# Optimization experiments

Measured on AMD Instinct MI355X. Metric: run time of the kernel, lower is better.

Reference implementation:

```python
import jax, jax.numpy as jnp
import numpy as np

B, S, E, H = 64, 512, 256, 512


def setup_inputs() -> dict:
    key = jax.random.key(0)
    ks = jax.random.split(key, 8)
    std_h = 1.0 / np.sqrt(H)
    std_e = 1.0 / np.sqrt(E)
    return {
        "inputs": jax.random.normal(ks[0], (B, S, E), dtype=jnp.float32),
        "timestamps": jax.random.uniform(ks[1], (B, S), dtype=jnp.float32) * 10.0,
        "W_all_w": jax.random.uniform(ks[2], (4 * H, H), jnp.float32, -std_h, std_h),
        "W_all_b": jax.random.uniform(ks[3], (4 * H,), jnp.float32, -std_h, std_h),
        "U_all_w": jax.random.uniform(ks[4], (4 * H, E), jnp.float32, -std_e, std_e),
        "U_all_b": jax.random.uniform(ks[5], (4 * H,), jnp.float32, -std_e, std_e),
        "W_d_w": jax.random.uniform(ks[6], (H, H), jnp.float32, -std_h, std_h),
        "W_d_b": jax.random.uniform(ks[7], (H,), jnp.float32, -std_h, std_h),
    }


def reference(inputs, timestamps, W_all_w, W_all_b, U_all_w, U_all_b, W_d_w, W_d_b):
    b, seq, embed = inputs.shape
    hidden = W_d_w.shape[0]
    # Precompute input projections for all steps: [b, seq, 4H]
    u_proj = jnp.einsum('bse,ge->bsg', inputs, U_all_w) + U_all_b
    # Time-decay factor per step: 1 / log(e + dt), shape [b, seq, 1]
    decay = (1.0 / jnp.log(jnp.float32(np.e) + timestamps))[..., None]

    def step(carry, xs):
        h, c = carry
        u_s, dec_s = xs  # [b, 4H], [b, 1]
        c_s1 = jnp.tanh(c @ W_d_w.T + W_d_b)
        c_adj = (c - c_s1) + c_s1 * dec_s
        outs = h @ W_all_w.T + W_all_b + u_s
        f, i, o, c_tmp = jnp.split(outs, 4, axis=1)
        f = jax.nn.sigmoid(f)
        i = jax.nn.sigmoid(i)
        o = jax.nn.sigmoid(o)
        c_tmp = jnp.tanh(c_tmp)
        c_new = f * c_adj + i * c_tmp
        h_new = o * jnp.tanh(c_new)
        return (h_new, c_new), h_new

    h0 = jnp.zeros((b, hidden), dtype=inputs.dtype)
    c0 = jnp.zeros((b, hidden), dtype=inputs.dtype)
    # scan over seq: move time to leading axis
    (h_f, c_f), hs = jax.lax.scan(
        step, (h0, c0),
        (jnp.swapaxes(u_proj, 0, 1), jnp.swapaxes(decay, 0, 1)))
    outputs = jnp.swapaxes(hs, 0, 1)  # [b, seq, H]
    return outputs, h_f, c_f
```

## Files before the change

kernel.cpp:

```cpp
#include <hip/hip_runtime.h>
#include <cmath>


typedef short bf16x8 __attribute__((ext_vector_type(8)));
typedef float f32x4  __attribute__((ext_vector_type(4)));

#define Bdim 64
#define Sdim 512
#define Edim 256
#define Hdim 512
#define NWG  64
#define NT   512
#define FSTR 16

#define WS_FLAGS 0
#define WS_HMIR0 16384
#define WS_HMIR1 (WS_HMIR0 + 65536)
#define WS_CMIR0 (WS_HMIR1 + 65536)
#define WS_CMIR1 (WS_CMIR0 + 65536)
#define WS_WFRAG (WS_CMIR1 + 65536)
#define WS_DFRAG (WS_WFRAG + 3145728)

__device__ __forceinline__ unsigned ld_dev_u32(const unsigned* p) {
    return __hip_atomic_load(p, __ATOMIC_RELAXED, __HIP_MEMORY_SCOPE_AGENT);
}
__device__ __forceinline__ void st_dev_u32(unsigned* p, unsigned v) {
    __hip_atomic_store(p, v, __ATOMIC_RELAXED, __HIP_MEMORY_SCOPE_AGENT);
}
__device__ __forceinline__ unsigned long long ld_dev_u64(const unsigned long long* p) {
    return __hip_atomic_load(p, __ATOMIC_RELAXED, __HIP_MEMORY_SCOPE_AGENT);
}
__device__ __forceinline__ unsigned short f2bf(float f) {
    union { float f; unsigned u; } v; v.f = f;
    return (unsigned short)((v.u + 0x7FFFu + ((v.u >> 16) & 1u)) >> 16);
}
__device__ __forceinline__ unsigned pack2(float lo, float hi) {
    return (unsigned)f2bf(lo) | ((unsigned)f2bf(hi) << 16);
}
__device__ __forceinline__ float fast_tanh(float x) {
    const float ax = __builtin_fabsf(x);
    const float e  = __expf(-2.0f * ax);
    const float t  = (1.0f - e) / (1.0f + e);
    return __builtin_copysignf(t, x);
}
__device__ __forceinline__ float fast_sigmoid(float x) {
    return 1.0f / (1.0f + __expf(-x));
}

__global__ __launch_bounds__(256) void tlstm_prep(
    const float* __restrict__ Wall, const float* __restrict__ Uall,
    const float* __restrict__ Wd, unsigned char* __restrict__ ws)
{
    const int w = blockIdx.x, t = threadIdx.x;
    unsigned short* Wfrag = (unsigned short*)(ws + WS_WFRAG);
    unsigned short* Dfrag = (unsigned short*)(ws + WS_DFRAG);
    const int l = t & 63, ks = t >> 6, nn = l & 15, q = l >> 4;

    if (w < 128) {
        const int cg = w >> 3, wv = w & 7;
        const int G = wv * 16 + nn, g = G >> 5, jj = G & 31;
        const int row = g * Hdim + cg * 32 + jj;
        for (int i = 0; i < 6; ++i) {
            const int kp = ks * 6 + i;
            const float* src = (kp < 16)
                ? Wall + (size_t)row * Hdim + kp * 32 + q * 8
                : Uall + (size_t)row * Edim + (kp - 16) * 32 + q * 8;
            unsigned* dst = (unsigned*)(Wfrag
                + (((size_t)(cg * 8 + wv) * 24 + kp) * 64 + l) * 8);
            #pragma unroll
            for (int p = 0; p < 4; ++p) dst[p] = pack2(src[2*p], src[2*p+1]);
        }
    } else if (w < 192) {
        const int u = w - 128, cg = u >> 2, q4 = u & 3;
        for (int half = 0; half < 2; ++half) {
            const int wv = q4 * 2 + half;
            const int i  = ks;
            const int dt = wv >> 2, kd = (wv & 3) * 4 + i;
            const int row = cg * 32 + dt * 16 + nn;
            const float* src = Wd + (size_t)row * Hdim + kd * 32 + q * 8;
            unsigned* dst = (unsigned*)(Dfrag
                + (((size_t)(cg * 8 + wv) * 4 + i) * 64 + l) * 8);
            #pragma unroll
            for (int p = 0; p < 4; ++p) dst[p] = pack2(src[2*p], src[2*p+1]);
        }
    } else {
        const int idx = (w - 192) * 256 + t;
        uint4* z = (uint4*)ws;
        for (int i = idx; i < 17408; i += 16384) z[i] = make_uint4(0, 0, 0, 0);
    }
}

__global__ __launch_bounds__(NT, 2) void tlstm_mfma(
    const float* __restrict__ x,
    const float* __restrict__ ts,
    const float* __restrict__ Wall_b,
    const float* __restrict__ Uall_b,
    const float* __restrict__ Wd_b,
    float* __restrict__ out,
    unsigned char* __restrict__ ws)
{
    __shared__ __align__(16) unsigned short h_sb[16 * 520];
    __shared__ __align__(16) unsigned short c_sb[16 * 520];
    __shared__ __align__(16) unsigned short x_sb[16 * 264];
    __shared__ float Dred[2][4][256];
    __shared__ float act[4 * 512];
    __shared__ float cs1v[512];
    __shared__ float decv[16];

    int* flags = (int*)(ws + WS_FLAGS);
    const unsigned short* Wfrag = (const unsigned short*)(ws + WS_WFRAG);
    const unsigned short* Dfrag = (const unsigned short*)(ws + WS_DFRAG);

    const int t    = threadIdx.x;
    const int bg   = blockIdx.x >> 4, cg = blockIdx.x & 15;
    const int b0   = bg * 16, j0 = cg * 32;
    const int w    = t >> 6, lane = t & 63, q = lane >> 4, nn = lane & 15;

    const int G = w * 16 + nn, g = G >> 5, jj = G & 31;
    const float bias_g = Wall_b[g * Hdim + j0 + jj] + Uall_b[g * Hdim + j0 + jj];
    const int rtl = t >> 8, rpos = t & 255, rm = rpos >> 4, rn = rpos & 15;
    const float bias_d = Wd_b[j0 + rtl * 16 + rn];
    const int fm = t >> 5, fj = t & 31;

    bf16x8 bw[24];
    #pragma unroll
    for (int i = 0; i < 24; ++i)
        bw[i] = *(const bf16x8*)(Wfrag
            + (((size_t)(cg * 8 + w) * 24 + i) * 64 + lane) * 8);
    bf16x8 bd[4];
    #pragma unroll
    for (int i = 0; i < 4; ++i)
        bd[i] = *(const bf16x8*)(Dfrag
            + (((size_t)(cg * 8 + w) * 4 + i) * 64 + lane) * 8);

    const int srow = t >> 5, sc32 = t & 31;

    auto stage_x = [&](int sx) {
        const float4* xp = (const float4*)(x + ((size_t)(b0 + srow) * Sdim + sx) * Edim + sc32 * 8);
        float4 v0 = xp[0], v1 = xp[1];
        *(uint4*)((unsigned*)x_sb + srow * 132 + sc32 * 4) =
            make_uint4(pack2(v0.x, v0.y), pack2(v0.z, v0.w),
                       pack2(v1.x, v1.y), pack2(v1.z, v1.w));
    };

    float c_reg = 0.0f;
    stage_x(0);

    for (int s = 0;; ++s) {
        {
            const unsigned long long* hsrc =
                (const unsigned long long*)(ws + WS_HMIR0 + (s & 1) * 65536);
            const unsigned long long* csrc =
                (const unsigned long long*)(ws + WS_CMIR0 + (s & 1) * 65536);
            const int goff = ((b0 + srow) * 256 + sc32 * 8) >> 1;
            unsigned long long hv[4], cv[4];
            #pragma unroll
            for (int i = 0; i < 4; ++i) hv[i] = ld_dev_u64(hsrc + goff + i);
            #pragma unroll
            for (int i = 0; i < 4; ++i) cv[i] = ld_dev_u64(csrc + goff + i);
            unsigned* hls = (unsigned*)h_sb + srow * 260 + sc32 * 8;
            unsigned* cls = (unsigned*)c_sb + srow * 260 + sc32 * 8;
            ((ulonglong2*)hls)[0] = make_ulonglong2(hv[0], hv[1]);
            ((ulonglong2*)hls)[1] = make_ulonglong2(hv[2], hv[3]);
            ((ulonglong2*)cls)[0] = make_ulonglong2(cv[0], cv[1]);
            ((ulonglong2*)cls)[1] = make_ulonglong2(cv[2], cv[3]);
        }
        __syncthreads();

        f32x4 acc0 = {0.f, 0.f, 0.f, 0.f}, acc1 = {0.f, 0.f, 0.f, 0.f};
        f32x4 accd = {0.f, 0.f, 0.f, 0.f};
        #pragma unroll
        for (int i = 0; i < 12; ++i) {
            bf16x8 av = *(const bf16x8*)(h_sb + nn * 520 + i * 32 + q * 8);
            acc0 = __builtin_amdgcn_mfma_f32_16x16x32_bf16(av, bw[i], acc0, 0, 0, 0);
        }
        #pragma unroll
        for (int i = 12; i < 24; ++i) {
            const unsigned short* asrc = (i < 16)
                ? (h_sb + nn * 520 + i * 32 + q * 8)
                : (x_sb + nn * 264 + (i - 16) * 32 + q * 8);
            bf16x8 av = *(const bf16x8*)asrc;
            acc1 = __builtin_amdgcn_mfma_f32_16x16x32_bf16(av, bw[i], acc1, 0, 0, 0);
        }
        #pragma unroll
        for (int i = 0; i < 4; ++i) {
            const int kd = (w & 3) * 4 + i;
            bf16x8 av = *(const bf16x8*)(c_sb + nn * 520 + kd * 32 + q * 8);
            accd = __builtin_amdgcn_mfma_f32_16x16x32_bf16(av, bd[i], accd, 0, 0, 0);
        }

        const int dt = w >> 2;
        #pragma unroll
        for (int r = 0; r < 4; ++r) {
            const int m = q * 4 + r;
            const float sv = acc0[r] + acc1[r] + bias_g;
            act[g * 512 + m * 32 + jj] = (g == 3) ? fast_tanh(sv) : fast_sigmoid(sv);
            Dred[dt][w & 3][m * 16 + ((nn + m) & 15)] = accd[r];
        }
        __syncthreads();

        {
            const int sl = rm * 16 + ((rn + rm) & 15);
            const float sv = Dred[rtl][0][sl] + Dred[rtl][1][sl]
                           + Dred[rtl][2][sl] + Dred[rtl][3][sl];
            cs1v[rm * 32 + rtl * 16 + rn] = fast_tanh(sv + bias_d);
        }
        if (t < 16)
            decv[t] = 1.0f / __logf(2.7182818284590452f + ts[(b0 + t) * Sdim + s]);
        __syncthreads();

        {
            const float dec  = decv[fm];
            const float cs1  = cs1v[t];
            const float cadj = (c_reg - cs1) + cs1 * dec;
            const float f  = act[t];
            const float ii = act[512 + t];
            const float oo = act[1024 + t];
            const float gg = act[1536 + t];
            const float cn = f * cadj + ii * gg;
            const float hn = oo * fast_tanh(cn);
            c_reg = cn;
            out[((size_t)(b0 + fm) * Sdim + s) * Hdim + j0 + fj] = hn;
            const float hn1 = __shfl_down(hn, 1);
            const float cn1 = __shfl_down(cn, 1);
            if (s < Sdim - 1) {
                if ((t & 1) == 0) {
                    unsigned* hmw = (unsigned*)(ws + WS_HMIR0 + ((s + 1) & 1) * 65536);
                    unsigned* cmw = (unsigned*)(ws + WS_CMIR0 + ((s + 1) & 1) * 65536);
                    const int didx = ((b0 + fm) * Hdim + j0 + fj) >> 1;
                    st_dev_u32(hmw + didx, pack2(hn, hn1));
                    st_dev_u32(cmw + didx, pack2(cn, cn1));
                }
            } else {
                float* hf = out + (size_t)Bdim * Sdim * Hdim;
                float* cf = hf + (size_t)Bdim * Hdim;
                hf[(b0 + fm) * Hdim + j0 + fj] = hn;
                cf[(b0 + fm) * Hdim + j0 + fj] = cn;
            }
        }

        if (s == Sdim - 1) break;

        __syncthreads();
        if (t == 0)
            __hip_atomic_store(&flags[blockIdx.x * FSTR], s + 1,
                               __ATOMIC_RELAXED, __HIP_MEMORY_SCOPE_AGENT);
        stage_x(s + 1);
        if (t < 16) {
            while (__hip_atomic_load(&flags[(bg * 16 + t) * FSTR],
                                     __ATOMIC_RELAXED,
                                     __HIP_MEMORY_SCOPE_AGENT) < s + 1) {
                __builtin_amdgcn_s_sleep(1);
            }
        }
        __syncthreads();
    }
}

extern "C" void kernel_launch(void* const* d_in, const int* in_sizes, int n_in,
                              void* d_out, int out_size, void* d_ws, size_t ws_size,
                              hipStream_t stream) {
    const float* x      = (const float*)d_in[0];
    const float* ts     = (const float*)d_in[1];
    const float* Wall   = (const float*)d_in[2];
    const float* Wall_b = (const float*)d_in[3];
    const float* Uall   = (const float*)d_in[4];
    const float* Uall_b = (const float*)d_in[5];
    const float* Wd     = (const float*)d_in[6];
    const float* Wd_b   = (const float*)d_in[7];

    tlstm_prep<<<256, 256, 0, stream>>>(Wall, Uall, Wd, (unsigned char*)d_ws);
    tlstm_mfma<<<NWG, NT, 0, stream>>>(x, ts, Wall_b, Uall_b, Wd_b,
                                       (float*)d_out, (unsigned char*)d_ws);
}
```

Measured before the change: 2.008 ms.

## Restructure per-step sync: per-producer flag waits, direct x MFMA, fewer barriers

```diff
diff --git a/kernel.cpp b/kernel.cpp
--- a/kernel.cpp
+++ b/kernel.cpp
@@ -99,13 +99,11 @@
     float* __restrict__ out,
     unsigned char* __restrict__ ws)
 {
-    __shared__ __align__(16) unsigned short h_sb[16 * 520];
-    __shared__ __align__(16) unsigned short c_sb[16 * 520];
-    __shared__ __align__(16) unsigned short x_sb[16 * 264];
+    __shared__ __align__(16) unsigned short h_sb[16 * 512];
+    __shared__ __align__(16) unsigned short c_sb[16 * 512];
     __shared__ float Dred[2][4][256];
     __shared__ float act[4 * 512];
-    __shared__ float cs1v[512];
-    __shared__ float decv[16];
+    __shared__ float dectab[16 * 512];
 
     int* flags = (int*)(ws + WS_FLAGS);
     const unsigned short* Wfrag = (const unsigned short*)(ws + WS_WFRAG);
@@ -118,9 +116,9 @@
 
     const int G = w * 16 + nn, g = G >> 5, jj = G & 31;
     const float bias_g = Wall_b[g * Hdim + j0 + jj] + Uall_b[g * Hdim + j0 + jj];
-    const int rtl = t >> 8, rpos = t & 255, rm = rpos >> 4, rn = rpos & 15;
-    const float bias_d = Wd_b[j0 + rtl * 16 + rn];
     const int fm = t >> 5, fj = t & 31;
+    const int fdt = fj >> 4, fn = fj & 15;
+    const float bias_d = Wd_b[j0 + fj];
 
     bf16x8 bw[24];
     #pragma unroll
@@ -134,58 +132,83 @@
             + (((size_t)(cg * 8 + w) * 4 + i) * 64 + lane) * 8);
 
     const int srow = t >> 5, sc32 = t & 31;
-
-    auto stage_x = [&](int sx) {
-        const float4* xp = (const float4*)(x + ((size_t)(b0 + srow) * Sdim + sx) * Edim + sc32 * 8);
-        float4 v0 = xp[0], v1 = xp[1];
-        *(uint4*)((unsigned*)x_sb + srow * 132 + sc32 * 4) =
-            make_uint4(pack2(v0.x, v0.y), pack2(v0.z, v0.w),
-                       pack2(v1.x, v1.y), pack2(v1.z, v1.w));
+    const int prod = sc32 >> 1;
+    const bool own = (prod == cg);
+
+    for (int i = t; i < 16 * Sdim; i += NT)
+        dectab[i] = 1.0f / __logf(2.7182818284590452f
+                                  + ts[(size_t)(b0 + (i >> 9)) * Sdim + (i & 511)]);
+
+    auto xmfma = [&](int sx) -> f32x4 {
+        f32x4 a = {0.f, 0.f, 0.f, 0.f};
+        const float* xb = x + ((size_t)(b0 + nn) * Sdim + sx) * Edim + q * 8;
+        #pragma unroll
+        for (int kk = 0; kk < 8; ++kk) {
+            float4 v0 = *(const float4*)(xb + kk * 32);
+            float4 v1 = *(const float4*)(xb + kk * 32 + 4);
+            union { unsigned u[4]; bf16x8 v; } cv;
+            asm("v_cvt_pk_bf16_f32 %0, %1, %2" : "=v"(cv.u[0]) : "v"(v0.x), "v"(v0.y));
+            asm("v_cvt_pk_bf16_f32 %0, %1, %2" : "=v"(cv.u[1]) : "v"(v0.z), "v"(v0.w));
+            asm("v_cvt_pk_bf16_f32 %0, %1, %2" : "=v"(cv.u[2]) : "v"(v1.x), "v"(v1.y));
+            asm("v_cvt_pk_bf16_f32 %0, %1, %2" : "=v"(cv.u[3]) : "v"(v1.z), "v"(v1.w));
+            a = __builtin_amdgcn_mfma_f32_16x16x32_bf16(cv.v, bw[16 + kk], a, 0, 0, 0);
+        }
+        return a;
     };
 
+    auto stage_hc = [&](int si) {
+        if (!own) {
+            const unsigned* fp = (const unsigned*)(flags + (bg * 16 + prod) * FSTR);
+            while ((int)ld_dev_u32(fp) < si) __builtin_amdgcn_s_sleep(1);
+        }
+        const unsigned long long* hsrc =
+            (const unsigned long long*)(ws + WS_HMIR0 + (si & 1) * 65536);
+        const unsigned long long* csrc =
+            (const unsigned long long*)(ws + WS_CMIR0 + (si & 1) * 65536);
+        const size_t goff = (size_t)(b0 + srow) * 128 + sc32 * 4;
+        unsigned long long hv[4], cv[4];
+        #pragma unroll
+        for (int i = 0; i < 4; ++i) hv[i] = ld_dev_u64(hsrc + goff + i);
+        #pragma unroll
+        for (int i = 0; i < 4; ++i) cv[i] = ld_dev_u64(csrc + goff + i);
+        const int p0 = (2 * sc32) ^ (srow & 7), p1 = (2 * sc32 + 1) ^ (srow & 7);
+        unsigned* hl = (unsigned*)h_sb + srow * 256;
+        unsigned* cl = (unsigned*)c_sb + srow * 256;
+        *(uint4*)(hl + p0 * 4) = make_uint4((unsigned)hv[0], (unsigned)(hv[0] >> 32),
+                                            (unsigned)hv[1], (unsigned)(hv[1] >> 32));
+        *(uint4*)(hl + p1 * 4) = make_uint4((unsigned)hv[2], (unsigned)(hv[2] >> 32),
+                                            (unsigned)hv[3], (unsigned)(hv[3] >> 32));
+        *(uint4*)(cl + p0 * 4) = make_uint4((unsigned)cv[0], (unsigned)(cv[0] >> 32),
+                                            (unsigned)cv[1], (unsigned)(cv[1] >> 32));
+        *(uint4*)(cl + p1 * 4) = make_uint4((unsigned)cv[2], (unsigned)(cv[2] >> 32),
+                                            (unsigned)cv[3], (unsigned)(cv[3] >> 32));
+    };
+
     float c_reg = 0.0f;
-    stage_x(0);
+    f32x4 accx = xmfma(0);
+    stage_hc(0);
+    __syncthreads();
 
     for (int s = 0;; ++s) {
-        {
-            const unsigned long long* hsrc =
-                (const unsigned long long*)(ws + WS_HMIR0 + (s & 1) * 65536);
-            const unsigned long long* csrc =
-                (const unsigned long long*)(ws + WS_CMIR0 + (s & 1) * 65536);
-            const int goff = ((b0 + srow) * 256 + sc32 * 8) >> 1;
-            unsigned long long hv[4], cv[4];
-            #pragma unroll
-            for (int i = 0; i < 4; ++i) hv[i] = ld_dev_u64(hsrc + goff + i);
-            #pragma unroll
-            for (int i = 0; i < 4; ++i) cv[i] = ld_dev_u64(csrc + goff + i);
-            unsigned* hls = (unsigned*)h_sb + srow * 260 + sc32 * 8;
-            unsigned* cls = (unsigned*)c_sb + srow * 260 + sc32 * 8;
-            ((ulonglong2*)hls)[0] = make_ulonglong2(hv[0], hv[1]);
-            ((ulonglong2*)hls)[1] = make_ulonglong2(hv[2], hv[3]);
-            ((ulonglong2*)cls)[0] = make_ulonglong2(cv[0], cv[1]);
-            ((ulonglong2*)cls)[1] = make_ulonglong2(cv[2], cv[3]);
-        }
-        __syncthreads();
-
         f32x4 acc0 = {0.f, 0.f, 0.f, 0.f}, acc1 = {0.f, 0.f, 0.f, 0.f};
         f32x4 accd = {0.f, 0.f, 0.f, 0.f};
         #pragma unroll
-        for (int i = 0; i < 12; ++i) {
-            bf16x8 av = *(const bf16x8*)(h_sb + nn * 520 + i * 32 + q * 8);
+        for (int i = 0; i < 8; ++i) {
+            bf16x8 av = *(const bf16x8*)(h_sb + nn * 512
+                + (((i * 4 + q) ^ (nn & 7)) * 8));
             acc0 = __builtin_amdgcn_mfma_f32_16x16x32_bf16(av, bw[i], acc0, 0, 0, 0);
         }
         #pragma unroll
-        for (int i = 12; i < 24; ++i) {
-            const unsigned short* asrc = (i < 16)
-                ? (h_sb + nn * 520 + i * 32 + q * 8)
-                : (x_sb + nn * 264 + (i - 16) * 32 + q * 8);
-            bf16x8 av = *(const bf16x8*)asrc;
+        for (int i = 8; i < 16; ++i) {
+            bf16x8 av = *(const bf16x8*)(h_sb + nn * 512
+                + (((i * 4 + q) ^ (nn & 7)) * 8));
             acc1 = __builtin_amdgcn_mfma_f32_16x16x32_bf16(av, bw[i], acc1, 0, 0, 0);
         }
         #pragma unroll
         for (int i = 0; i < 4; ++i) {
             const int kd = (w & 3) * 4 + i;
-            bf16x8 av = *(const bf16x8*)(c_sb + nn * 520 + kd * 32 + q * 8);
+            bf16x8 av = *(const bf16x8*)(c_sb + nn * 512
+                + (((kd * 4 + q) ^ (nn & 7)) * 8));
             accd = __builtin_amdgcn_mfma_f32_16x16x32_bf16(av, bd[i], accd, 0, 0, 0);
         }
 
@@ -193,34 +216,28 @@
         #pragma unroll
         for (int r = 0; r < 4; ++r) {
             const int m = q * 4 + r;
-            const float sv = acc0[r] + acc1[r] + bias_g;
-            act[g * 512 + m * 32 + jj] = (g == 3) ? fast_tanh(sv) : fast_sigmoid(sv);
+            const float sv = acc0[r] + acc1[r] + accx[r] + bias_g;
+            act[g * 512 + m * 32 + ((jj + m) & 31)] =
+                (g == 3) ? fast_tanh(sv) : fast_sigmoid(sv);
             Dred[dt][w & 3][m * 16 + ((nn + m) & 15)] = accd[r];
         }
         __syncthreads();
 
         {
-            const int sl = rm * 16 + ((rn + rm) & 15);
-            const float sv = Dred[rtl][0][sl] + Dred[rtl][1][sl]
-                           + Dred[rtl][2][sl] + Dred[rtl][3][sl];
-            cs1v[rm * 32 + rtl * 16 + rn] = fast_tanh(sv + bias_d);
-        }
-        if (t < 16)
-            decv[t] = 1.0f / __logf(2.7182818284590452f + ts[(b0 + t) * Sdim + s]);
-        __syncthreads();
-
-        {
-            const float dec  = decv[fm];
-            const float cs1  = cs1v[t];
+            const int sl = fm * 16 + ((fn + fm) & 15);
+            const float dsum = Dred[fdt][0][sl] + Dred[fdt][1][sl]
+                             + Dred[fdt][2][sl] + Dred[fdt][3][sl];
+            const float cs1  = fast_tanh(dsum + bias_d);
+            const float dec  = dectab[fm * 512 + s];
             const float cadj = (c_reg - cs1) + cs1 * dec;
-            const float f  = act[t];
-            const float ii = act[512 + t];
-            const float oo = act[1024 + t];
-            const float gg = act[1536 + t];
+            const int   ai   = fm * 32 + ((fj + fm) & 31);
+            const float f  = act[ai];
+            const float ii = act[512 + ai];
+            const float oo = act[1024 + ai];
+            const float gg = act[1536 + ai];
             const float cn = f * cadj + ii * gg;
             const float hn = oo * fast_tanh(cn);
             c_reg = cn;
-            out[((size_t)(b0 + fm) * Sdim + s) * Hdim + j0 + fj] = hn;
             const float hn1 = __shfl_down(hn, 1);
             const float cn1 = __shfl_down(cn, 1);
             if (s < Sdim - 1) {
@@ -237,22 +254,18 @@
                 hf[(b0 + fm) * Hdim + j0 + fj] = hn;
                 cf[(b0 + fm) * Hdim + j0 + fj] = cn;
             }
+            out[((size_t)(b0 + fm) * Sdim + s) * Hdim + j0 + fj] = hn;
         }
 
         if (s == Sdim - 1) break;
 
+        asm volatile("s_waitcnt vmcnt(0)" ::: "memory");
         __syncthreads();
         if (t == 0)
-            __hip_atomic_store(&flags[blockIdx.x * FSTR], s + 1,
-                               __ATOMIC_RELAXED, __HIP_MEMORY_SCOPE_AGENT);
-        stage_x(s + 1);
-        if (t < 16) {
-            while (__hip_atomic_load(&flags[(bg * 16 + t) * FSTR],
-                                     __ATOMIC_RELAXED,
-                                     __HIP_MEMORY_SCOPE_AGENT) < s + 1) {
-                __builtin_amdgcn_s_sleep(1);
-            }
-        }
+            st_dev_u32((unsigned*)(flags + blockIdx.x * FSTR), (unsigned)(s + 1));
+
+        accx = xmfma(s + 1);
+        stage_hc(s + 1);
         __syncthreads();
     }
 }
```

Measured after the change: 3.551 ms. 1.77x slower.

## Ping-pong two batch halves per workgroup to overlap recurrence sync with compute

Applied to the files above, without the earlier changes.

```diff
diff --git a/kernel.cpp b/kernel.cpp
--- a/kernel.cpp
+++ b/kernel.cpp
@@ -9,7 +9,7 @@
 #define Sdim 512
 #define Edim 256
 #define Hdim 512
-#define NWG  64
+#define NWG  32
 #define NT   512
 #define FSTR 16
 
@@ -90,7 +90,7 @@
     }
 }
 
-__global__ __launch_bounds__(NT, 2) void tlstm_mfma(
+__global__ __launch_bounds__(NT, 1) void tlstm_mfma(
     const float* __restrict__ x,
     const float* __restrict__ ts,
     const float* __restrict__ Wall_b,
@@ -99,12 +99,11 @@
     float* __restrict__ out,
     unsigned char* __restrict__ ws)
 {
-    __shared__ __align__(16) unsigned short h_sb[16 * 520];
-    __shared__ __align__(16) unsigned short c_sb[16 * 520];
-    __shared__ __align__(16) unsigned short x_sb[16 * 264];
+    __shared__ __align__(16) unsigned short h_sb[2][16 * 520];
+    __shared__ __align__(16) unsigned short c_sb[2][16 * 520];
+    __shared__ __align__(16) unsigned short x_sb[2][16 * 264];
     __shared__ float Dred[2][4][256];
     __shared__ float act[4 * 512];
-    __shared__ float cs1v[512];
     __shared__ float decv[16];
 
     int* flags = (int*)(ws + WS_FLAGS);
@@ -113,14 +112,14 @@
 
     const int t    = threadIdx.x;
     const int bg   = blockIdx.x >> 4, cg = blockIdx.x & 15;
-    const int b0   = bg * 16, j0 = cg * 32;
+    const int b0   = bg * 32, j0 = cg * 32;
     const int w    = t >> 6, lane = t & 63, q = lane >> 4, nn = lane & 15;
 
     const int G = w * 16 + nn, g = G >> 5, jj = G & 31;
     const float bias_g = Wall_b[g * Hdim + j0 + jj] + Uall_b[g * Hdim + j0 + jj];
-    const int rtl = t >> 8, rpos = t & 255, rm = rpos >> 4, rn = rpos & 15;
-    const float bias_d = Wd_b[j0 + rtl * 16 + rn];
     const int fm = t >> 5, fj = t & 31;
+    const int fdt = fj >> 4, fn = fj & 15;
+    const float bias_d = Wd_b[j0 + fj];
 
     bf16x8 bw[24];
     #pragma unroll
@@ -135,125 +134,139 @@
 
     const int srow = t >> 5, sc32 = t & 31;
 
-    auto stage_x = [&](int sx) {
-        const float4* xp = (const float4*)(x + ((size_t)(b0 + srow) * Sdim + sx) * Edim + sc32 * 8);
+    for (int i = t; i < 16 * 520; i += NT) { h_sb[0][i] = 0; c_sb[0][i] = 0; }
+    {
+        const float4* xp = (const float4*)(x + ((size_t)(b0 + srow) * Sdim + 0) * Edim + sc32 * 8);
         float4 v0 = xp[0], v1 = xp[1];
-        *(uint4*)((unsigned*)x_sb + srow * 132 + sc32 * 4) =
+        *(uint4*)((unsigned*)&x_sb[0][0] + srow * 132 + sc32 * 4) =
             make_uint4(pack2(v0.x, v0.y), pack2(v0.z, v0.w),
                        pack2(v1.x, v1.y), pack2(v1.z, v1.w));
-    };
-
-    float c_reg = 0.0f;
-    stage_x(0);
+    }
+    float c_reg0 = 0.0f, c_reg1 = 0.0f;
+    __syncthreads();
 
     for (int s = 0;; ++s) {
-        {
-            const unsigned long long* hsrc =
-                (const unsigned long long*)(ws + WS_HMIR0 + (s & 1) * 65536);
-            const unsigned long long* csrc =
-                (const unsigned long long*)(ws + WS_CMIR0 + (s & 1) * 65536);
-            const int goff = ((b0 + srow) * 256 + sc32 * 8) >> 1;
+        #pragma unroll
+        for (int r = 0; r < 2; ++r) {
+            const int rb0 = b0 + r * 16;
+            const unsigned short* hb = &h_sb[r][0];
+            const unsigned short* cb = &c_sb[r][0];
+            const unsigned short* xb = &x_sb[r][0];
+
+            f32x4 acc0 = {0.f, 0.f, 0.f, 0.f}, acc1 = {0.f, 0.f, 0.f, 0.f};
+            f32x4 accd = {0.f, 0.f, 0.f, 0.f};
+            #pragma unroll
+            for (int i = 0; i < 12; ++i) {
+                bf16x8 av = *(const bf16x8*)(hb + nn * 520 + i * 32 + q * 8);
+                acc0 = __builtin_amdgcn_mfma_f32_16x16x32_bf16(av, bw[i], acc0, 0, 0, 0);
+            }
+            #pragma unroll
+            for (int i = 12; i < 24; ++i) {
+                const unsigned short* asrc = (i < 16)
+                    ? (hb + nn * 520 + i * 32 + q * 8)
+                    : (xb + nn * 264 + (i - 16) * 32 + q * 8);
+                bf16x8 av = *(const bf16x8*)asrc;
+                acc1 = __builtin_amdgcn_mfma_f32_16x16x32_bf16(av, bw[i], acc1, 0, 0, 0);
+            }
+            #pragma unroll
+            for (int i = 0; i < 4; ++i) {
+                const int kd = (w & 3) * 4 + i;
+                bf16x8 av = *(const bf16x8*)(cb + nn * 520 + kd * 32 + q * 8);
+                accd = __builtin_amdgcn_mfma_f32_16x16x32_bf16(av, bd[i], accd, 0, 0, 0);
+            }
+
+            const int dt = w >> 2;
+            #pragma unroll
+            for (int rr = 0; rr < 4; ++rr) {
+                const int m = q * 4 + rr;
+                const float sv = acc0[rr] + acc1[rr] + bias_g;
+                act[g * 512 + m * 32 + jj] =
+                    (g == 3) ? fast_tanh(sv) : fast_sigmoid(sv);
+                Dred[dt][w & 3][m * 16 + ((nn + m) & 15)] = accd[rr];
+            }
+            if (t < 16)
+                decv[t] = 1.0f / __logf(2.7182818284590452f
+                                        + ts[(size_t)(rb0 + t) * Sdim + s]);
+
+            const int nr = 1 - r, ns = s + r;
+            const bool do_stage = (ns < Sdim);
+            if (do_stage && t < 16) {
+                const unsigned* fp = (const unsigned*)&flags[(bg * 16 + t) * FSTR + nr];
+                while ((int)ld_dev_u32(fp) < ns) __builtin_amdgcn_s_sleep(1);
+            }
+            __syncthreads();
+
             unsigned long long hv[4], cv[4];
-            #pragma unroll
-            for (int i = 0; i < 4; ++i) hv[i] = ld_dev_u64(hsrc + goff + i);
-            #pragma unroll
-            for (int i = 0; i < 4; ++i) cv[i] = ld_dev_u64(csrc + goff + i);
-            unsigned* hls = (unsigned*)h_sb + srow * 260 + sc32 * 8;
-            unsigned* cls = (unsigned*)c_sb + srow * 260 + sc32 * 8;
-            ((ulonglong2*)hls)[0] = make_ulonglong2(hv[0], hv[1]);
-            ((ulonglong2*)hls)[1] = make_ulonglong2(hv[2], hv[3]);
-            ((ulonglong2*)cls)[0] = make_ulonglong2(cv[0], cv[1]);
-            ((ulonglong2*)cls)[1] = make_ulonglong2(cv[2], cv[3]);
+            float4 xv0, xv1;
+            if (do_stage) {
+                const unsigned long long* hsrc =
+                    (const unsigned long long*)(ws + WS_HMIR0 + (ns & 1) * 65536);
+                const unsigned long long* csrc =
+                    (const unsigned long long*)(ws + WS_CMIR0 + (ns & 1) * 65536);
+                const size_t goff = (size_t)(b0 + nr * 16 + srow) * 128 + sc32 * 4;
+                #pragma unroll
+                for (int i = 0; i < 4; ++i) hv[i] = ld_dev_u64(hsrc + goff + i);
+                #pragma unroll
+                for (int i = 0; i < 4; ++i) cv[i] = ld_dev_u64(csrc + goff + i);
+                const float4* xp = (const float4*)(x
+                    + ((size_t)(b0 + nr * 16 + srow) * Sdim + ns) * Edim + sc32 * 8);
+                xv0 = xp[0]; xv1 = xp[1];
+            }
+
+            {
+                const int sl = fm * 16 + ((fn + fm) & 15);
+                const float dsum = Dred[fdt][0][sl] + Dred[fdt][1][sl]
+                                 + Dred[fdt][2][sl] + Dred[fdt][3][sl];
+                const float cs1  = fast_tanh(dsum + bias_d);
+                const float dec  = decv[fm];
+                const float cp   = r ? c_reg1 : c_reg0;
+                const float cadj = (cp - cs1) + cs1 * dec;
+                const float f  = act[t];
+                const float ii = act[512 + t];
+                const float oo = act[1024 + t];
+                const float gg = act[1536 + t];
+                const float cn = f * cadj + ii * gg;
+                const float hn = oo * fast_tanh(cn);
+                if (r) c_reg1 = cn; else c_reg0 = cn;
+                out[((size_t)(rb0 + fm) * Sdim + s) * Hdim + j0 + fj] = hn;
+                const float hn1 = __shfl_down(hn, 1);
+                const float cn1 = __shfl_down(cn, 1);
+                if (s < Sdim - 1) {
+                    if ((t & 1) == 0) {
+                        unsigned* hmw = (unsigned*)(ws + WS_HMIR0 + ((s + 1) & 1) * 65536);
+                        unsigned* cmw = (unsigned*)(ws + WS_CMIR0 + ((s + 1) & 1) * 65536);
+                        const int didx = ((rb0 + fm) * Hdim + j0 + fj) >> 1;
+                        st_dev_u32(hmw + didx, pack2(hn, hn1));
+                        st_dev_u32(cmw + didx, pack2(cn, cn1));
+                    }
+                } else {
+                    float* hf = out + (size_t)Bdim * Sdim * Hdim;
+                    float* cf = hf + (size_t)Bdim * Hdim;
+                    hf[(rb0 + fm) * Hdim + j0 + fj] = hn;
+                    cf[(rb0 + fm) * Hdim + j0 + fj] = cn;
+                }
+            }
+
+            if (s == Sdim - 1 && r == 1) return;
+
+            asm volatile("s_waitcnt vmcnt(0)" ::: "memory");
+            __syncthreads();
+            if (t == 0 && s < Sdim - 1)
+                st_dev_u32((unsigned*)&flags[(bg * 16 + cg) * FSTR + r],
+                           (unsigned)(s + 1));
+            if (do_stage) {
+                unsigned* hls = (unsigned*)&h_sb[nr][0] + srow * 260 + sc32 * 8;
+                unsigned* cls = (unsigned*)&c_sb[nr][0] + srow * 260 + sc32 * 8;
+                ((ulonglong2*)hls)[0] = make_ulonglong2(hv[0], hv[1]);
+                ((ulonglong2*)hls)[1] = make_ulonglong2(hv[2], hv[3]);
+                ((ulonglong2*)cls)[0] = make_ulonglong2(cv[0], cv[1]);
+                ((ulonglong2*)cls)[1] = make_ulonglong2(cv[2], cv[3]);
+                *(uint4*)((unsigned*)&x_sb[nr][0] + srow * 132 + sc32 * 4) =
+                    make_uint4(pack2(xv0.x, xv0.y), pack2(xv0.z, xv0.w),
+                               pack2(xv1.x, xv1.y), pack2(xv1.z, xv1.w));
+            }
+            __syncthreads();
         }
-        __syncthreads();
-
-        f32x4 acc0 = {0.f, 0.f, 0.f, 0.f}, acc1 = {0.f, 0.f, 0.f, 0.f};
-        f32x4 accd = {0.f, 0.f, 0.f, 0.f};
-        #pragma unroll
-        for (int i = 0; i < 12; ++i) {
-            bf16x8 av = *(const bf16x8*)(h_sb + nn * 520 + i * 32 + q * 8);
-            acc0 = __builtin_amdgcn_mfma_f32_16x16x32_bf16(av, bw[i], acc0, 0, 0, 0);
-        }
-        #pragma unroll
-        for (int i = 12; i < 24; ++i) {
-            const unsigned short* asrc = (i < 16)
-                ? (h_sb + nn * 520 + i * 32 + q * 8)
-                : (x_sb + nn * 264 + (i - 16) * 32 + q * 8);
-            bf16x8 av = *(const bf16x8*)asrc;
-            acc1 = __builtin_amdgcn_mfma_f32_16x16x32_bf16(av, bw[i], acc1, 0, 0, 0);
-        }
-        #pragma unroll
-        for (int i = 0; i < 4; ++i) {
-            const int kd = (w & 3) * 4 + i;
-            bf16x8 av = *(const bf16x8*)(c_sb + nn * 520 + kd * 32 + q * 8);
-            accd = __builtin_amdgcn_mfma_f32_16x16x32_bf16(av, bd[i], accd, 0, 0, 0);
-        }
-
-        const int dt = w >> 2;
-        #pragma unroll
-        for (int r = 0; r < 4; ++r) {
-            const int m = q * 4 + r;
-            const float sv = acc0[r] + acc1[r] + bias_g;
-            act[g * 512 + m * 32 + jj] = (g == 3) ? fast_tanh(sv) : fast_sigmoid(sv);
-            Dred[dt][w & 3][m * 16 + ((nn + m) & 15)] = accd[r];
-        }
-        __syncthreads();
-
-        {
-            const int sl = rm * 16 + ((rn + rm) & 15);
-            const float sv = Dred[rtl][0][sl] + Dred[rtl][1][sl]
-                           + Dred[rtl][2][sl] + Dred[rtl][3][sl];
-            cs1v[rm * 32 + rtl * 16 + rn] = fast_tanh(sv + bias_d);
-        }
-        if (t < 16)
-            decv[t] = 1.0f / __logf(2.7182818284590452f + ts[(b0 + t) * Sdim + s]);
-        __syncthreads();
-
-        {
-            const float dec  = decv[fm];
-            const float cs1  = cs1v[t];
-            const float cadj = (c_reg - cs1) + cs1 * dec;
-            const float f  = act[t];
-            const float ii = act[512 + t];
-            const float oo = act[1024 + t];
-            const float gg = act[1536 + t];
-            const float cn = f * cadj + ii * gg;
-            const float hn = oo * fast_tanh(cn);
-            c_reg = cn;
-            out[((size_t)(b0 + fm) * Sdim + s) * Hdim + j0 + fj] = hn;
-            const float hn1 = __shfl_down(hn, 1);
-            const float cn1 = __shfl_down(cn, 1);
-            if (s < Sdim - 1) {
-                if ((t & 1) == 0) {
-                    unsigned* hmw = (unsigned*)(ws + WS_HMIR0 + ((s + 1) & 1) * 65536);
-                    unsigned* cmw = (unsigned*)(ws + WS_CMIR0 + ((s + 1) & 1) * 65536);
-                    const int didx = ((b0 + fm) * Hdim + j0 + fj) >> 1;
-                    st_dev_u32(hmw + didx, pack2(hn, hn1));
-                    st_dev_u32(cmw + didx, pack2(cn, cn1));
-                }
-            } else {
-                float* hf = out + (size_t)Bdim * Sdim * Hdim;
-                float* cf = hf + (size_t)Bdim * Hdim;
-                hf[(b0 + fm) * Hdim + j0 + fj] = hn;
-                cf[(b0 + fm) * Hdim + j0 + fj] = cn;
-            }
-        }
-
-        if (s == Sdim - 1) break;
-
-        __syncthreads();
-        if (t == 0)
-            __hip_atomic_store(&flags[blockIdx.x * FSTR], s + 1,
-                               __ATOMIC_RELAXED, __HIP_MEMORY_SCOPE_AGENT);
-        stage_x(s + 1);
-        if (t < 16) {
-            while (__hip_atomic_load(&flags[(bg * 16 + t) * FSTR],
-                                     __ATOMIC_RELAXED,
-                                     __HIP_MEMORY_SCOPE_AGENT) < s + 1) {
-                __builtin_amdgcn_s_sleep(1);
-            }
-        }
-        __syncthreads();
     }
 }
 
```

Measured after the change: 4.171 ms. +107.7%, slower.

## Replace block-wide flag barrier with per-wave flag waits and precompute decay table

Applied to the files above, without the earlier changes.

```diff
diff --git a/kernel.cpp b/kernel.cpp
--- a/kernel.cpp
+++ b/kernel.cpp
@@ -104,8 +104,7 @@
     __shared__ __align__(16) unsigned short x_sb[16 * 264];
     __shared__ float Dred[2][4][256];
     __shared__ float act[4 * 512];
-    __shared__ float cs1v[512];
-    __shared__ float decv[16];
+    __shared__ float dectab[16 * 512];
 
     int* flags = (int*)(ws + WS_FLAGS);
     const unsigned short* Wfrag = (const unsigned short*)(ws + WS_WFRAG);
@@ -118,9 +117,9 @@
 
     const int G = w * 16 + nn, g = G >> 5, jj = G & 31;
     const float bias_g = Wall_b[g * Hdim + j0 + jj] + Uall_b[g * Hdim + j0 + jj];
-    const int rtl = t >> 8, rpos = t & 255, rm = rpos >> 4, rn = rpos & 15;
-    const float bias_d = Wd_b[j0 + rtl * 16 + rn];
     const int fm = t >> 5, fj = t & 31;
+    const int fdt = fj >> 4, fn = fj & 15;
+    const float bias_d = Wd_b[j0 + fj];
 
     bf16x8 bw[24];
     #pragma unroll
@@ -143,30 +142,40 @@
                        pack2(v1.x, v1.y), pack2(v1.z, v1.w));
     };
 
+    const int mrow = lane & 15, seg = lane >> 4;
+    auto stage_hc = [&](int si) {
+        const unsigned* f0 = (const unsigned*)&flags[(bg * 16 + 2 * w) * FSTR];
+        const unsigned* f1 = (const unsigned*)&flags[(bg * 16 + 2 * w + 1) * FSTR];
+        while ((int)ld_dev_u32(f0) < si) __builtin_amdgcn_s_sleep(1);
+        while ((int)ld_dev_u32(f1) < si) __builtin_amdgcn_s_sleep(1);
+        const unsigned long long* hsrc =
+            (const unsigned long long*)(ws + WS_HMIR0 + (si & 1) * 65536);
+        const unsigned long long* csrc =
+            (const unsigned long long*)(ws + WS_CMIR0 + (si & 1) * 65536);
+        const size_t goff = (size_t)(b0 + mrow) * 128 + w * 16 + seg * 4;
+        unsigned long long hv[4], cv[4];
+        #pragma unroll
+        for (int i = 0; i < 4; ++i) hv[i] = ld_dev_u64(hsrc + goff + i);
+        #pragma unroll
+        for (int i = 0; i < 4; ++i) cv[i] = ld_dev_u64(csrc + goff + i);
+        unsigned* hl = (unsigned*)h_sb + mrow * 260 + (w * 16 + seg * 4) * 2;
+        unsigned* cl = (unsigned*)c_sb + mrow * 260 + (w * 16 + seg * 4) * 2;
+        ((ulonglong2*)hl)[0] = make_ulonglong2(hv[0], hv[1]);
+        ((ulonglong2*)hl)[1] = make_ulonglong2(hv[2], hv[3]);
+        ((ulonglong2*)cl)[0] = make_ulonglong2(cv[0], cv[1]);
+        ((ulonglong2*)cl)[1] = make_ulonglong2(cv[2], cv[3]);
+    };
+
+    for (int i = t; i < 16 * 520; i += NT) { h_sb[i] = 0; c_sb[i] = 0; }
+    for (int i = t; i < 16 * Sdim; i += NT)
+        dectab[i] = 1.0f / __logf(2.7182818284590452f
+                                  + ts[(size_t)(b0 + (i >> 9)) * Sdim + (i & 511)]);
+    stage_x(0);
     float c_reg = 0.0f;
-    stage_x(0);
+    float hn_keep = 0.0f; size_t out_idx = 0;
+    __syncthreads();
 
     for (int s = 0;; ++s) {
-        {
-            const unsigned long long* hsrc =
-                (const unsigned long long*)(ws + WS_HMIR0 + (s & 1) * 65536);
-            const unsigned long long* csrc =
-                (const unsigned long long*)(ws + WS_CMIR0 + (s & 1) * 65536);
-            const int goff = ((b0 + srow) * 256 + sc32 * 8) >> 1;
-            unsigned long long hv[4], cv[4];
-            #pragma unroll
-            for (int i = 0; i < 4; ++i) hv[i] = ld_dev_u64(hsrc + goff + i);
-            #pragma unroll
-            for (int i = 0; i < 4; ++i) cv[i] = ld_dev_u64(csrc + goff + i);
-            unsigned* hls = (unsigned*)h_sb + srow * 260 + sc32 * 8;
-            unsigned* cls = (unsigned*)c_sb + srow * 260 + sc32 * 8;
-            ((ulonglong2*)hls)[0] = make_ulonglong2(hv[0], hv[1]);
-            ((ulonglong2*)hls)[1] = make_ulonglong2(hv[2], hv[3]);
-            ((ulonglong2*)cls)[0] = make_ulonglong2(cv[0], cv[1]);
-            ((ulonglong2*)cls)[1] = make_ulonglong2(cv[2], cv[3]);
-        }
-        __syncthreads();
-
         f32x4 acc0 = {0.f, 0.f, 0.f, 0.f}, acc1 = {0.f, 0.f, 0.f, 0.f};
         f32x4 accd = {0.f, 0.f, 0.f, 0.f};
         #pragma unroll
@@ -191,27 +200,21 @@
 
         const int dt = w >> 2;
         #pragma unroll
-        for (int r = 0; r < 4; ++r) {
-            const int m = q * 4 + r;
-            const float sv = acc0[r] + acc1[r] + bias_g;
-            act[g * 512 + m * 32 + jj] = (g == 3) ? fast_tanh(sv) : fast_sigmoid(sv);
-            Dred[dt][w & 3][m * 16 + ((nn + m) & 15)] = accd[r];
+        for (int rr = 0; rr < 4; ++rr) {
+            const int m = q * 4 + rr;
+            const float sv = acc0[rr] + acc1[rr] + bias_g;
+            act[g * 512 + m * 32 + jj] =
+                (g == 3) ? fast_tanh(sv) : fast_sigmoid(sv);
+            Dred[dt][w & 3][m * 16 + ((nn + m) & 15)] = accd[rr];
         }
         __syncthreads();
 
         {
-            const int sl = rm * 16 + ((rn + rm) & 15);
-            const float sv = Dred[rtl][0][sl] + Dred[rtl][1][sl]
-                           + Dred[rtl][2][sl] + Dred[rtl][3][sl];
-            cs1v[rm * 32 + rtl * 16 + rn] = fast_tanh(sv + bias_d);
-        }
-        if (t < 16)
-            decv[t] = 1.0f / __logf(2.7182818284590452f + ts[(b0 + t) * Sdim + s]);
-        __syncthreads();
-
-        {
-            const float dec  = decv[fm];
-            const float cs1  = cs1v[t];
+            const int sl = fm * 16 + ((fn + fm) & 15);
+            const float dsum = Dred[fdt][0][sl] + Dred[fdt][1][sl]
+                             + Dred[fdt][2][sl] + Dred[fdt][3][sl];
+            const float cs1  = fast_tanh(dsum + bias_d);
+            const float dec  = dectab[fm * 512 + s];
             const float cadj = (c_reg - cs1) + cs1 * dec;
             const float f  = act[t];
             const float ii = act[512 + t];
@@ -220,7 +223,8 @@
             const float cn = f * cadj + ii * gg;
             const float hn = oo * fast_tanh(cn);
             c_reg = cn;
-            out[((size_t)(b0 + fm) * Sdim + s) * Hdim + j0 + fj] = hn;
+            hn_keep = hn;
+            out_idx = ((size_t)(b0 + fm) * Sdim + s) * Hdim + j0 + fj;
             const float hn1 = __shfl_down(hn, 1);
             const float cn1 = __shfl_down(cn, 1);
             if (s < Sdim - 1) {
@@ -232,6 +236,7 @@
                     st_dev_u32(cmw + didx, pack2(cn, cn1));
                 }
             } else {
+                out[out_idx] = hn;
                 float* hf = out + (size_t)Bdim * Sdim * Hdim;
                 float* cf = hf + (size_t)Bdim * Hdim;
                 hf[(b0 + fm) * Hdim + j0 + fj] = hn;
@@ -243,16 +248,11 @@
 
         __syncthreads();
         if (t == 0)
-            __hip_atomic_store(&flags[blockIdx.x * FSTR], s + 1,
-                               __ATOMIC_RELAXED, __HIP_MEMORY_SCOPE_AGENT);
+            st_dev_u32((unsigned*)&flags[(bg * 16 + cg) * FSTR],
+                       (unsigned)(s + 1));
+        out[out_idx] = hn_keep;
         stage_x(s + 1);
-        if (t < 16) {
-            while (__hip_atomic_load(&flags[(bg * 16 + t) * FSTR],
-                                     __ATOMIC_RELAXED,
-                                     __HIP_MEMORY_SCOPE_AGENT) < s + 1) {
-                __builtin_amdgcn_s_sleep(1);
-            }
-        }
+        stage_hc(s + 1);
         __syncthreads();
     }
 }
```

Result: slower. 2.436 ms (+21.3%).
